# Kernel tuning notes

Measured on AMD Instinct MI355X. Metric: run time of the kernel, lower is better.

The kernel has to match this reference:

```python
import jax, jax.numpy as jnp
import numpy as np

DECAY = 0.999
EPS = 1e-05
COMMITMENT_COST = 0.25
M, D = 1024, 256
B, H, W = 32, 32, 32


def setup_inputs() -> dict:
    key = jax.random.key(0)
    k1, k2 = jax.random.split(key)
    init_bound = 1.0 / M
    x = jax.random.normal(k1, (B, H, W, D), dtype=jnp.float32)
    embedding = jax.random.uniform(k2, (M, D), dtype=jnp.float32,
                                   minval=-init_bound, maxval=init_bound)
    ema_count = jnp.zeros((M,), dtype=jnp.float32)
    ema_weight = embedding  # buffer initialized as embedding.clone()
    return {"x": x, "embedding": embedding, "ema_count": ema_count,
            "ema_weight": ema_weight}


def reference(x, embedding, ema_count, ema_weight):
    Mn, Dn = embedding.shape
    x_flat = jax.lax.stop_gradient(x).reshape(-1, Dn)          # [N, D]
    N = x_flat.shape[0]

    # (-cdist)^2 == squared euclidean distance; argmin is the same.
    x_sq = jnp.sum(x_flat * x_flat, axis=-1, keepdims=True)    # [N, 1]
    e_sq = jnp.sum(embedding * embedding, axis=-1)             # [M]
    distances = x_sq - 2.0 * (x_flat @ embedding.T) + e_sq[None, :]  # [N, M]
    indices = jnp.argmin(distances, axis=-1)                   # [N]

    quantized = embedding[indices].reshape(x.shape)            # gather

    # one-hot column sums == scatter-add of ones; encodings.T @ x_flat == scatter-add rows
    counts = jnp.zeros((Mn,), x.dtype).at[indices].add(1.0)    # [M]
    dw = jnp.zeros((Mn, Dn), x.dtype).at[indices].add(x_flat)  # [M, D]

    new_count = DECAY * ema_count + (1.0 - DECAY) * counts
    n = jnp.sum(new_count)
    new_count = (new_count + EPS) / (n + Mn * EPS) * n
    new_weight = DECAY * ema_weight + (1.0 - DECAY) * dw
    new_embedding = new_weight / new_count[:, None]

    codebook_loss = jnp.mean((jax.lax.stop_gradient(x) - quantized) ** 2)
    e_latent_loss = jnp.mean((x - jax.lax.stop_gradient(quantized)) ** 2)
    commitment_loss = COMMITMENT_COST * e_latent_loss

    quantized_st = x + jax.lax.stop_gradient(quantized - x)    # straight-through

    avg_probs = counts / N
    perplexity = jnp.exp(-jnp.sum(avg_probs * jnp.log(avg_probs + 1e-10)))

    return (quantized_st, commitment_loss, codebook_loss, perplexity,
            new_embedding, new_count, new_weight)
```

## Files before the change

kernel.cpp:

```cpp
#include <hip/hip_runtime.h>
#include <cfloat>
#include <math.h>

#define N_TOK 32768
#define DIM   256
#define MCODE 1024

typedef unsigned short u16;
typedef unsigned long long u64;
typedef __attribute__((ext_vector_type(8))) _Float16 h16x8;
typedef __attribute__((ext_vector_type(8))) short short8;
typedef __attribute__((ext_vector_type(4))) float f32x4;

constexpr float DECAY_ = 0.999f;
constexpr float OMD_   = (float)(1.0 - 0.999);
constexpr float EPS_   = 1e-5f;
constexpr float MEPS_  = (float)(1024 * 1e-5);

constexpr int WS_EH   = 0;
constexpr int WS_ESQ  = 262144;
constexpr int WS_CNTI = 263168;
constexpr int WS_BI   = 264192;
constexpr int WS_LP   = 296960;
constexpr int WS_KEY  = 299008;

constexpr int OUT_Q        = 0;
constexpr int OUT_COMMIT   = 8388608;
constexpr int OUT_CODEBOOK = 8388609;
constexpr int OUT_PERP     = 8388610;
constexpr int OUT_NE       = 8388611;
constexpr int OUT_NC       = 8650755;
constexpr int OUT_NW       = 8651779;

static __device__ __forceinline__ void gl2lds16(const u16* g, char* l) {
    __builtin_amdgcn_global_load_lds(
        (const __attribute__((address_space(1))) unsigned int*)g,
        (__attribute__((address_space(3))) unsigned int*)l, 16, 0, 0);
}
static __device__ __forceinline__ unsigned fmap(float f) {
    unsigned u = __float_as_uint(f);
    return (u & 0x80000000u) ? ~u : (u | 0x80000000u);
}

static __device__ __forceinline__ void pack8_lin(const float* __restrict__ src,
                                                 u16* __restrict__ dst,
                                                 size_t i8, float scale) {
    float4 v0 = *(const float4*)&src[i8];
    float4 v1 = *(const float4*)&src[i8 + 4];
    h16x8 hv;
    hv[0]=(_Float16)(v0.x*scale); hv[1]=(_Float16)(v0.y*scale);
    hv[2]=(_Float16)(v0.z*scale); hv[3]=(_Float16)(v0.w*scale);
    hv[4]=(_Float16)(v1.x*scale); hv[5]=(_Float16)(v1.y*scale);
    hv[6]=(_Float16)(v1.z*scale); hv[7]=(_Float16)(v1.w*scale);
    *(h16x8*)&dst[i8] = hv;
}

__global__ __launch_bounds__(256) void vq_setup(const float* __restrict__ x,
                                                const float* __restrict__ emb,
                                                u16* __restrict__ xh,
                                                u16* __restrict__ eh,
                                                float* __restrict__ esq,
                                                u64* __restrict__ keys,
                                                int* __restrict__ cnti) {
    const int b = blockIdx.x, tid = threadIdx.x;
    if (b < 4096) {
        pack8_lin(x, xh, (size_t)b * 2048 + tid * 8, 1.0f);
        return;
    }
    const int p = b - 4096;
    const int lane = tid & 63, w = tid >> 6;
    if (p < 128) {
        pack8_lin(emb, eh, (size_t)p * 2048 + tid * 8, 1024.0f);
    } else if (p < 384) {
        int c = (p - 128) * 4 + w;
        float4 v = *(const float4*)&emb[c * DIM + lane * 4];
        float s = v.x * v.x + v.y * v.y + v.z * v.z + v.w * v.w;
#pragma unroll
        for (int off = 32; off; off >>= 1) s += __shfl_xor(s, off, 64);
        if (lane == 0) esq[c] = s;
    } else if (p < 512) {
        keys[(p - 384) * 256 + tid] = ~0ULL;
    } else {
#pragma unroll
        for (int i = 0; i < 4; ++i) cnti[i * 256 + tid] = 0;
    }
}

__global__ __launch_bounds__(256) void vq_scores_mfma(const u16* __restrict__ xh,
                                                      const u16* __restrict__ eh,
                                                      const float* __restrict__ esq,
                                                      u64* __restrict__ keys) {
    __shared__ __align__(16) char smem[33792];
    const int tid  = threadIdx.x;
    const int lane = tid & 63, w = tid >> 6;
    const int wm = w & 1, wn = w >> 1;
    const int raw = blockIdx.x;
    const int rb = (raw >> 6) * 8 + (raw & 7);
    const int cs = (raw >> 3) & 7;

    const u16* gb0 = xh + (size_t)rb * 32768;
    const u16* gb1 = eh + (size_t)cs * 32768;

    const h16x8* Ah = (const h16x8*)(smem);
    const h16x8* Bh = (const h16x8*)(smem + 8192);

    const int ln16 = lane & 15, q4 = lane >> 4;

    f32x4 acc[4][4];
#pragma unroll
    for (int i = 0; i < 4; ++i)
#pragma unroll
        for (int j = 0; j < 4; ++j) acc[i][j] = (f32x4)0.f;

    for (int kc = 0; kc < 8; ++kc) {
        __syncthreads();
#pragma unroll
        for (int j = 0; j < 4; ++j) {
            int t = w * 4 + j;
            int arr = t >> 3, slot = t & 7;
            const u16* g = (arr == 0 ? gb0 : gb1)
                           + (slot * 16 + ln16) * 256 + kc * 32 + q4 * 8;
            gl2lds16(g, smem + arr * 8192 + slot * 1024);
        }
        __syncthreads();

        h16x8 ah[4];
#pragma unroll
        for (int tm = 0; tm < 4; ++tm)
            ah[tm] = Ah[(wm * 4 + tm) * 64 + lane];
#pragma unroll
        for (int tn = 0; tn < 4; ++tn) {
            h16x8 bh = Bh[(wn * 4 + tn) * 64 + lane];
#pragma unroll
            for (int tm = 0; tm < 4; ++tm) {
                acc[tm][tn] = __builtin_amdgcn_mfma_f32_16x16x32_f16(ah[tm], bh, acc[tm][tn], 0, 0, 0);
            }
        }
    }

    __syncthreads();
    float* cv = (float*)smem;
    int*   ci = (int*)(smem + 16896);
#pragma unroll
    for (int tm = 0; tm < 4; ++tm) {
        float bv[4];
        int   bi[4];
#pragma unroll
        for (int r = 0; r < 4; ++r) { bv[r] = FLT_MAX; bi[r] = 0; }
#pragma unroll
        for (int tn = 0; tn < 4; ++tn) {
            int c = cs * 128 + wn * 64 + tn * 16 + ln16;
            float ec = esq[c];
#pragma unroll
            for (int r = 0; r < 4; ++r) {
                float d = fmaf(-0.001953125f, acc[tm][tn][r], ec);
                if (d < bv[r]) { bv[r] = d; bi[r] = c; }
            }
        }
        int row0 = wm * 64 + tm * 16 + q4 * 4;
        int slot = wn * 16 + ln16;
#pragma unroll
        for (int r = 0; r < 4; ++r) {
            cv[(row0 + r) * 33 + slot] = bv[r];
            ci[(row0 + r) * 33 + slot] = bi[r];
        }
    }
    __syncthreads();
    if (tid < 128) {
        float bv = cv[tid * 33];
        int   bi = ci[tid * 33];
#pragma unroll
        for (int s = 1; s < 32; ++s) {
            float v = cv[tid * 33 + s];
            int  ix = ci[tid * 33 + s];
            if (v < bv || (v == bv && ix < bi)) { bv = v; bi = ix; }
        }
        u64 key = ((u64)fmap(bv) << 32) | (unsigned)bi;
        atomicMin(&keys[rb * 128 + tid], key);
    }
}

__global__ __launch_bounds__(256) void vq_quant(const float* __restrict__ x,
                                                const float* __restrict__ emb,
                                                const u64* __restrict__ keys,
                                                float* __restrict__ outq,
                                                int* __restrict__ cnti,
                                                int* __restrict__ bi_arr,
                                                float* __restrict__ lpart) {
    const int tid = threadIdx.x, lane = tid & 63, w = tid >> 6;
    const float4* x4 = (const float4*)x;
    const float4* e4 = (const float4*)emb;
    float4* o4 = (float4*)outq;
    float lacc = 0.f;
#pragma unroll
    for (int it = 0; it < 4; ++it) {
        int row = blockIdx.x * 16 + it * 4 + w;
        int bi = (int)(unsigned)(keys[row] & 0xffffffffULL);
        if (lane == 0) { atomicAdd(&cnti[bi], 1); bi_arr[row] = bi; }
        float4 xv = x4[row * 64 + lane];
        float4 ev = e4[bi * 64 + lane];
        float4 q;
        q.x = xv.x + (ev.x - xv.x);  q.y = xv.y + (ev.y - xv.y);
        q.z = xv.z + (ev.z - xv.z);  q.w = xv.w + (ev.w - xv.w);
        o4[row * 64 + lane] = q;
        float dx = xv.x - ev.x, dy = xv.y - ev.y, dz = xv.z - ev.z, dwv = xv.w - ev.w;
        lacc += dx * dx + dy * dy + dz * dz + dwv * dwv;
    }
#pragma unroll
    for (int off = 32; off; off >>= 1) lacc += __shfl_xor(lacc, off, 64);
    __shared__ float red[4];
    if (lane == 0) red[w] = lacc;
    __syncthreads();
    if (tid == 0) lpart[blockIdx.x] = red[0] + red[1] + red[2] + red[3];
}

#define MEGA_CAP 6144
__global__ __launch_bounds__(256) void vq_mega(const float* __restrict__ x,
                                               const float* __restrict__ ema_count,
                                               const float* __restrict__ ema_weight,
                                               const int* __restrict__ cnti,
                                               const int* __restrict__ bi_arr,
                                               const float* __restrict__ lpart,
                                               float* __restrict__ out) {
    const int m = blockIdx.x, tid = threadIdx.x;
    __shared__ float fs[256];
    __shared__ int list[MEGA_CAP];
    __shared__ int lcount;

    float rsum = 0.f;
#pragma unroll
    for (int i = 0; i < 4; ++i) rsum += ema_count[tid * 4 + i];
    fs[tid] = rsum;
    if (tid == 0) lcount = 0;
    __syncthreads();
    for (int s = 128; s; s >>= 1) { if (tid < s) fs[tid] += fs[tid + s]; __syncthreads(); }
    const float n = DECAY_ * fs[0] + OMD_ * (float)N_TOK;
    __syncthreads();

    const int4* b4 = (const int4*)bi_arr;
#pragma unroll 4
    for (int i = tid; i < N_TOK / 4; i += 256) {
        int4 v = b4[i];
        if (v.x == m) { int p = atomicAdd(&lcount, 1); if (p < MEGA_CAP) list[p] = 4 * i; }
        if (v.y == m) { int p = atomicAdd(&lcount, 1); if (p < MEGA_CAP) list[p] = 4 * i + 1; }
        if (v.z == m) { int p = atomicAdd(&lcount, 1); if (p < MEGA_CAP) list[p] = 4 * i + 2; }
        if (v.w == m) { int p = atomicAdd(&lcount, 1); if (p < MEGA_CAP) list[p] = 4 * i + 3; }
    }
    __syncthreads();
    const int nm = lcount;
    float dwsum;
    if (nm <= MEGA_CAP) {
        float a0 = 0.f, a1 = 0.f, a2 = 0.f, a3 = 0.f;
        int i = 0;
        for (; i + 4 <= nm; i += 4) {
            a0 += x[list[i]     * DIM + tid];
            a1 += x[list[i + 1] * DIM + tid];
            a2 += x[list[i + 2] * DIM + tid];
            a3 += x[list[i + 3] * DIM + tid];
        }
        for (; i < nm; ++i) a0 += x[list[i] * DIM + tid];
        dwsum = (a0 + a1) + (a2 + a3);
    } else {
        __shared__ int chunk[256];
        float a0 = 0.f;
        for (int base = 0; base < N_TOK; base += 256) {
            __syncthreads();
            chunk[tid] = bi_arr[base + tid];
            __syncthreads();
            for (int j = 0; j < 256; ++j)
                if (chunk[j] == m) a0 += x[(base + j) * DIM + tid];
        }
        dwsum = a0;
    }

    float raw_m = DECAY_ * ema_count[m] + OMD_ * (float)nm;
    float ncm = (raw_m + EPS_) / (n + MEPS_) * n;
    float nw = DECAY_ * ema_weight[m * DIM + tid] + OMD_ * dwsum;
    out[OUT_NW + m * DIM + tid] = nw;
    out[OUT_NE + m * DIM + tid] = nw / ncm;
    if (tid == 0) out[OUT_NC + m] = ncm;

    if (m == 0) {
        float ent = 0.f;
#pragma unroll
        for (int i = 0; i < 4; ++i) {
            float p = (float)cnti[tid * 4 + i] / (float)N_TOK;
            ent += p * logf(p + 1e-10f);
        }
        __syncthreads();
        fs[tid] = ent;
        __syncthreads();
        for (int s = 128; s; s >>= 1) { if (tid < s) fs[tid] += fs[tid + s]; __syncthreads(); }
        float entr = fs[0];
        __syncthreads();
        float ls = 0.f;
#pragma unroll
        for (int k = 0; k < 8; ++k) ls += lpart[tid + 256 * k];
        fs[tid] = ls;
        __syncthreads();
        for (int s = 128; s; s >>= 1) { if (tid < s) fs[tid] += fs[tid + s]; __syncthreads(); }
        if (tid == 0) {
            float mean = fs[0] / (float)(N_TOK * DIM);
            out[OUT_COMMIT]   = 0.25f * mean;
            out[OUT_CODEBOOK] = mean;
            out[OUT_PERP]     = expf(-entr);
        }
    }
}

extern "C" void kernel_launch(void* const* d_in, const int* in_sizes, int n_in,
                              void* d_out, int out_size, void* d_ws, size_t ws_size,
                              hipStream_t stream) {
    const float* x          = (const float*)d_in[0];
    const float* emb        = (const float*)d_in[1];
    const float* ema_count  = (const float*)d_in[2];
    const float* ema_weight = (const float*)d_in[3];
    float* out = (float*)d_out;
    float* wf  = (float*)d_ws;

    u16* xh = (u16*)d_out;
    u16* eh = (u16*)(wf + WS_EH);

    float* esq    = wf + WS_ESQ;
    int*   cnti   = (int*)(wf + WS_CNTI);
    int*   bi_arr = (int*)(wf + WS_BI);
    float* lpart  = wf + WS_LP;
    u64*   keys   = (u64*)(wf + WS_KEY);

    vq_setup<<<4609, 256, 0, stream>>>(x, emb, xh, eh, esq, keys, cnti);
    vq_scores_mfma<<<2048, 256, 0, stream>>>(xh, eh, esq, keys);
    vq_quant<<<2048, 256, 0, stream>>>(x, emb, keys, out, cnti, bi_arr, lpart);
    vq_mega<<<MCODE, 256, 0, stream>>>(x, ema_count, ema_weight, cnti, bi_arr,
                                       lpart, out);
}
```

Baseline: 164.9 us.

## Load MFMA operands directly from global memory instead of staging through LDS

The score GEMM no longer stages x and codebook tiles into shared memory with global_load_lds and two barriers per k-chunk. Each wave now loads its own fp16 fragments straight from global memory into registers, and the k loop is fully unrolled so the compiler can issue loads early. This removes the per-chunk barriers and LDS traffic. In exchange each tile is fetched twice, once by each of the two waves that need it, so global and L2 traffic doubles, and register pressure rises from the unrolled loads.

```diff
diff --git a/kernel.cpp b/kernel.cpp
--- a/kernel.cpp
+++ b/kernel.cpp
@@ -9,7 +9,6 @@
 typedef unsigned short u16;
 typedef unsigned long long u64;
 typedef __attribute__((ext_vector_type(8))) _Float16 h16x8;
-typedef __attribute__((ext_vector_type(8))) short short8;
 typedef __attribute__((ext_vector_type(4))) float f32x4;
 
 constexpr float DECAY_ = 0.999f;
@@ -32,11 +31,6 @@
 constexpr int OUT_NC       = 8650755;
 constexpr int OUT_NW       = 8651779;
 
-static __device__ __forceinline__ void gl2lds16(const u16* g, char* l) {
-    __builtin_amdgcn_global_load_lds(
-        (const __attribute__((address_space(1))) unsigned int*)g,
-        (__attribute__((address_space(3))) unsigned int*)l, 16, 0, 0);
-}
 static __device__ __forceinline__ unsigned fmap(float f) {
     unsigned u = __float_as_uint(f);
     return (u & 0x80000000u) ? ~u : (u | 0x80000000u);
@@ -97,45 +91,37 @@
     const int raw = blockIdx.x;
     const int rb = (raw >> 6) * 8 + (raw & 7);
     const int cs = (raw >> 3) & 7;
-
-    const u16* gb0 = xh + (size_t)rb * 32768;
-    const u16* gb1 = eh + (size_t)cs * 32768;
-
-    const h16x8* Ah = (const h16x8*)(smem);
-    const h16x8* Bh = (const h16x8*)(smem + 8192);
-
     const int ln16 = lane & 15, q4 = lane >> 4;
 
+    const u16* ab[4];
+    const u16* bb[4];
+#pragma unroll
+    for (int t = 0; t < 4; ++t) {
+        int arow = rb * 128 + wm * 64 + t * 16 + ln16;
+        ab[t] = xh + (size_t)arow * DIM + q4 * 8;
+        int bcol = cs * 128 + wn * 64 + t * 16 + ln16;
+        bb[t] = eh + (size_t)bcol * DIM + q4 * 8;
+    }
+
     f32x4 acc[4][4];
 #pragma unroll
     for (int i = 0; i < 4; ++i)
 #pragma unroll
         for (int j = 0; j < 4; ++j) acc[i][j] = (f32x4)0.f;
 
+#pragma unroll
     for (int kc = 0; kc < 8; ++kc) {
-        __syncthreads();
-#pragma unroll
-        for (int j = 0; j < 4; ++j) {
-            int t = w * 4 + j;
-            int arr = t >> 3, slot = t & 7;
-            const u16* g = (arr == 0 ? gb0 : gb1)
-                           + (slot * 16 + ln16) * 256 + kc * 32 + q4 * 8;
-            gl2lds16(g, smem + arr * 8192 + slot * 1024);
-        }
-        __syncthreads();
-
-        h16x8 ah[4];
-#pragma unroll
-        for (int tm = 0; tm < 4; ++tm)
-            ah[tm] = Ah[(wm * 4 + tm) * 64 + lane];
-#pragma unroll
-        for (int tn = 0; tn < 4; ++tn) {
-            h16x8 bh = Bh[(wn * 4 + tn) * 64 + lane];
-#pragma unroll
-            for (int tm = 0; tm < 4; ++tm) {
-                acc[tm][tn] = __builtin_amdgcn_mfma_f32_16x16x32_f16(ah[tm], bh, acc[tm][tn], 0, 0, 0);
-            }
-        }
+        h16x8 ah[4], bh[4];
+#pragma unroll
+        for (int t = 0; t < 4; ++t) {
+            ah[t] = *(const h16x8*)(ab[t] + kc * 32);
+            bh[t] = *(const h16x8*)(bb[t] + kc * 32);
+        }
+#pragma unroll
+        for (int tn = 0; tn < 4; ++tn)
+#pragma unroll
+            for (int tm = 0; tm < 4; ++tm)
+                acc[tm][tn] = __builtin_amdgcn_mfma_f32_16x16x32_f16(ah[tm], bh[tn], acc[tm][tn], 0, 0, 0);
     }
 
     __syncthreads();
```

New measurement: 187.3 us. 13.6% more time.
